# Optimization experiments

Hardware: AMD Instinct MI355X
Metric: run time of the kernel (lower is better)

## Reference

```python
import jax, jax.numpy as jnp
import numpy as np

B, C, H, W = 16, 1536, 32, 32
M = 64      # num_clusters
L = 128     # cluster_dim
G = 256     # token_dim
HID = 512
OT_ITERS = 3
EPS = 1e-6


def setup_inputs() -> dict:
    key = jax.random.key(0)
    ks = jax.random.split(key, 12)
    def w(k, shape, fan_in):
        return jax.random.normal(k, shape, jnp.float32) * (1.0 / np.sqrt(fan_in))
    return {
        'x': jax.random.normal(ks[0], (B, C, H, W), jnp.float32),
        't': jax.random.normal(ks[1], (B, C), jnp.float32),
        # token_features: Linear(C->512), ReLU, Linear(512->G)
        'Wt1': w(ks[2], (HID, C), C), 'bt1': jnp.zeros((HID,), jnp.float32),
        'Wt2': w(ks[3], (G, HID), HID), 'bt2': jnp.zeros((G,), jnp.float32),
        # cluster_features: 1x1 Conv(C->512), ReLU, 1x1 Conv(512->L)
        'Wc1': w(ks[4], (HID, C), C), 'bc1': jnp.zeros((HID,), jnp.float32),
        'Wc2': w(ks[5], (L, HID), HID), 'bc2': jnp.zeros((L,), jnp.float32),
        # score: 1x1 Conv(C->512), ReLU, 1x1 Conv(512->M)
        'Ws1': w(ks[6], (HID, C), C), 'bs1': jnp.zeros((HID,), jnp.float32),
        'Ws2': w(ks[7], (M, HID), HID), 'bs2': jnp.zeros((M,), jnp.float32),
        # temp_predictor: Conv1d(L->1, k=1)
        'Wtp': w(ks[8], (L,), L), 'btp': jnp.zeros((), jnp.float32),
        'dust_bin': jnp.asarray(1.0, jnp.float32),
        'burst_b': jnp.asarray(0.0, jnp.float32),
        'burst_p': jnp.asarray(1.0, jnp.float32),
        'lambda_discount': jnp.asarray(0.5, jnp.float32),
    }


def _log_optimal_transport(scores, alpha, iters):
    # scores: [B, m, n]; alpha: scalar dust-bin logit
    b, m, n = scores.shape
    Z0 = jnp.concatenate([scores, jnp.broadcast_to(alpha, (b, 1, n))], axis=1)  # [B, m+1, n]
    norm = -jnp.log(jnp.asarray(m + n, scores.dtype))
    log_mu = jnp.concatenate([jnp.full((m,), norm, scores.dtype),
                              (jnp.log(jnp.asarray(n, scores.dtype)) + norm)[None]])  # [m+1]
    log_nu = jnp.full((n,), norm, scores.dtype)
    u = jnp.zeros((b, m + 1), scores.dtype)
    v = jnp.zeros((b, n), scores.dtype)
    for _ in range(iters):
        u = log_mu - jax.nn.logsumexp(Z0 + v[:, None, :], axis=2)
        v = log_nu - jax.nn.logsumexp(Z0 + u[:, :, None], axis=1)
    return Z0 + u[:, :, None] + v[:, None, :] - norm


def _l2norm(a, axis):
    return a / jnp.maximum(jnp.linalg.norm(a, axis=axis, keepdims=True), 1e-12)


def _forward(x, t, Wt1, bt1, Wt2, bt2, Wc1, bc1, Wc2, bc2, Ws1, bs1, Ws2, bs2,
             Wtp, btp, dust_bin, burst_b, burst_p, lambda_discount):
    b, c, h, w = x.shape
    n = h * w
    xf = x.reshape(b, c, n)  # [B, C, N] (1x1 convs == per-pixel MLP)
    # cluster features f: [B, L, N]
    h1 = jax.nn.relu(jnp.einsum('bcn,oc->bon', xf, Wc1) + bc1[:, None])
    f = jnp.einsum('bhn,lh->bln', h1, Wc2) + bc2[:, None]
    # assignment scores p: [B, M, N]
    h2 = jax.nn.relu(jnp.einsum('bcn,oc->bon', xf, Ws1) + bs1[:, None])
    p = jnp.einsum('bhn,mh->bmn', h2, Ws2) + bs2[:, None]
    # global token: [B, G]
    tok = jax.nn.relu(t @ Wt1.T + bt1) @ Wt2.T + bt2
    # Sinkhorn OT soft assignment, drop dust bin row
    P = jnp.exp(_log_optimal_transport(p, dust_bin, OT_ITERS))[:, :-1, :]  # [B, M, N]
    # burst-aware weighting
    f_norm = _l2norm(f, axis=1)                                  # [B, L, N]
    T_i = jax.nn.softplus(jnp.einsum('bln,l->bn', f, Wtp) + btp)  # [B, N]
    sim = jnp.einsum('bli,blj->bij', f_norm, f_norm)              # [B, N, N]
    T_avg = (T_i[:, :, None] + T_i[:, None, :]) * 0.5
    burst_w = jax.nn.sigmoid(T_avg * sim + burst_b)
    discount = jnp.clip(jnp.sum(burst_w, axis=-1) ** burst_p, 1e-3, 1e3)  # [B, N]
    lam = jax.nn.sigmoid(lambda_discount)
    P_adj = (1.0 - lam) * P + lam * (P / (discount[:, None, :] + EPS))
    # local aggregation: (f[:, :, None, :] * P[:, None, :, :]).sum(-1) == batched matmul
    agg = jnp.einsum('bln,bmn->blm', f, P_adj)  # [B, L, M]
    agg = _l2norm(agg, axis=1).reshape(b, -1)   # [B, L*M]
    tok_n = _l2norm(tok, axis=-1)
    g = jnp.concatenate([tok_n, agg], axis=-1)  # [B, G + L*M]
    return _l2norm(g, axis=-1)


def reference(x, t, Wt1, bt1, Wt2, bt2, Wc1, bc1, Wc2, bc2, Ws1, bs1, Ws2, bs2,
              Wtp, btp, dust_bin, burst_b, burst_p, lambda_discount):
    return _forward(x, t, Wt1, bt1, Wt2, bt2, Wc1, bc1, Wc2, bc2, Ws1, bs1, Ws2, bs2,
                    Wtp, btp, dust_bin, burst_b, burst_p, lambda_discount)
```

## Files before the change

### kernel.cpp

```cpp
#include <hip/hip_runtime.h>
#include <math.h>

#define B_   16
#define C_   1536
#define N_   1024
#define M_   64
#define L_   128
#define G_   256
#define HID_ 512

typedef __attribute__((ext_vector_type(8))) short short8;
typedef __attribute__((ext_vector_type(4))) float floatx4;

__device__ __forceinline__ unsigned short f2bf_rne(float x) {
    unsigned u = __float_as_uint(x);
    unsigned r = u + 0x7fffu + ((u >> 16) & 1u);
    return (unsigned short)(r >> 16);
}
__device__ __forceinline__ unsigned pack_bf2(float lo, float hi) {
    unsigned a = __float_as_uint(lo) + 0x8000u;
    unsigned b = __float_as_uint(hi) + 0x8000u;
    return (a >> 16) | (b & 0xffff0000u);
}
__device__ __forceinline__ float bf2f(unsigned short u) {
    return __uint_as_float(((unsigned)u) << 16);
}
__device__ __forceinline__ void gl2lds16(const void* g, void* l) {
    __builtin_amdgcn_global_load_lds(
        (const __attribute__((address_space(1))) void*)g,
        (__attribute__((address_space(3))) void*)l, 16, 0, 0);
}

__global__ __launch_bounds__(256) void cast_w_kernel(
    const float* __restrict__ Wc1, const float* __restrict__ Ws1,
    const float* __restrict__ Wc2, const float* __restrict__ Ws2,
    unsigned short* __restrict__ Wbf, unsigned short* __restrict__ W2,
    float* __restrict__ agg, float* __restrict__ draw,
    float* __restrict__ rowsum)
{
    const int T1 = 1024 * 1536;
    const int T2 = 192 * 1024;
    int idx = blockIdx.x * 256 + threadIdx.x;
    if (idx < T1) {
        float v = (idx < 512 * 1536) ? Wc1[idx] : Ws1[idx - 512 * 1536];
        Wbf[idx] = f2bf_rne(v);
    } else if (idx < T1 + T2) {
        int i2 = idx - T1;
        int row = i2 >> 10, k = i2 & 1023;
        float v = 0.f;
        if (row < 128) { if (k < 512) v = Wc2[row * 512 + k]; }
        else           { if (k >= 512) v = Ws2[(row - 128) * 512 + (k - 512)]; }
        W2[i2] = f2bf_rne(v);
    } else {
        int zi = idx - (T1 + T2);
        if (zi < 131072) agg[zi] = 0.f;
        else if (zi < 131072 + 16384) draw[zi - 131072] = 0.f;
        else if (zi < 131072 + 16384 + 1040) rowsum[zi - 131072 - 16384] = 0.f;
    }
}

__global__ __launch_bounds__(256) void xt_kernel(
    const float* __restrict__ x, unsigned short* __restrict__ xT)
{
    __shared__ float Xs[64][65];
    const int t = threadIdx.x;
    const int n0 = blockIdx.x * 64, c0 = blockIdx.y * 64, b = blockIdx.z;
    const float* xb = x + (long)b * C_ * N_;
    #pragma unroll
    for (int it = 0; it < 16; ++it) {
        int idx = it * 256 + t, cr = idx >> 6, nc = idx & 63;
        Xs[cr][nc] = xb[(long)(c0 + cr) * N_ + n0 + nc];
    }
    __syncthreads();
    unsigned* xo = (unsigned*)(xT + (long)b * N_ * C_);
    #pragma unroll
    for (int it = 0; it < 8; ++it) {
        int idx = it * 256 + t, nr = idx >> 5, pc = idx & 31;
        xo[(long)(n0 + nr) * 768 + (c0 >> 1) + pc] =
            pack_bf2(Xs[2 * pc][nr], Xs[2 * pc + 1][nr]);
    }
}

__global__ __launch_bounds__(256, 2) void gemm1_kernel(
    const unsigned short* __restrict__ Wbf, const unsigned short* __restrict__ xT,
    const float* __restrict__ bc1, const float* __restrict__ bs1,
    unsigned short* __restrict__ hT)
{
    __shared__ unsigned short sh[8704];
    unsigned short* As = sh;
    unsigned short* Bs = sh + 4096;
    const int t = threadIdx.x;
    const int lane = t & 63, w = t >> 6;
    const int n0 = blockIdx.x * 128, o0 = blockIdx.y * 128, b = blockIdx.z;
    const unsigned short* xb = xT + (long)b * N_ * C_;

    const int wo = (w >> 1) * 64, wn = (w & 1) * 64;
    const int lrow = lane & 15, kgrp = lane >> 4;
    const int arow = t >> 2, acol = (t & 3) * 8;

    floatx4 acc[4][4];
    #pragma unroll
    for (int i = 0; i < 4; ++i)
        #pragma unroll
        for (int j = 0; j < 4; ++j) acc[i][j] = (floatx4)0.0f;

    for (int k0 = 0; k0 < C_; k0 += 32) {
        #pragma unroll
        for (int r = 0; r < 2; ++r)
            gl2lds16(Wbf + (long)(o0 + r * 64 + arow) * C_ + k0 + acol,
                     (char*)As + r * 4096 + t * 16);
        #pragma unroll
        for (int r = 0; r < 2; ++r)
            gl2lds16(xb + (long)(n0 + r * 64 + arow) * C_ + k0 + acol,
                     (char*)Bs + r * 4096 + t * 16);
        __syncthreads();
        short8 af[4], bfr[4];
        #pragma unroll
        for (int i = 0; i < 4; ++i)
            af[i] = *(const short8*)((const char*)As +
                        (wo + i * 16 + lrow) * 64 + kgrp * 16);
        #pragma unroll
        for (int j = 0; j < 4; ++j)
            bfr[j] = *(const short8*)((const char*)Bs +
                        (wn + j * 16 + lrow) * 64 + kgrp * 16);
        #pragma unroll
        for (int i = 0; i < 4; ++i)
            #pragma unroll
            for (int j = 0; j < 4; ++j)
                acc[i][j] = __builtin_amdgcn_mfma_f32_16x16x32_bf16(
                    af[i], bfr[j], acc[i][j], 0, 0, 0);
        __syncthreads();
    }

    const float* bias = (o0 < 512) ? bc1 : bs1;
    const int ob = (o0 < 512) ? o0 : o0 - 512;
    for (int half = 0; half < 2; ++half) {
        if ((w & 1) == half) {
            #pragma unroll
            for (int i = 0; i < 4; ++i) {
                int o_loc = wo + i * 16 + kgrp * 4;
                float b0 = bias[ob + o_loc + 0], b1 = bias[ob + o_loc + 1];
                float b2 = bias[ob + o_loc + 2], b3 = bias[ob + o_loc + 3];
                #pragma unroll
                for (int j = 0; j < 4; ++j) {
                    int n_loc = j * 16 + lrow;
                    float v0 = fmaxf(acc[i][j][0] + b0, 0.f);
                    float v1 = fmaxf(acc[i][j][1] + b1, 0.f);
                    float v2 = fmaxf(acc[i][j][2] + b2, 0.f);
                    float v3 = fmaxf(acc[i][j][3] + b3, 0.f);
                    uint2 pk;
                    pk.x = pack_bf2(v0, v1) & 0u;
                    pk.x = ((unsigned)f2bf_rne(v0)) | (((unsigned)f2bf_rne(v1)) << 16);
                    pk.y = ((unsigned)f2bf_rne(v2)) | (((unsigned)f2bf_rne(v3)) << 16);
                    *(uint2*)((char*)sh + n_loc * 272 + o_loc * 2) = pk;
                }
            }
        }
        __syncthreads();
        #pragma unroll
        for (int ps = 0; ps < 4; ++ps) {
            int n_loc = ps * 16 + (t >> 4);
            int o8 = (t & 15) * 8;
            uint4 q = *(const uint4*)((const char*)sh + n_loc * 272 + o8 * 2);
            *(uint4*)&hT[((long)b * N_ + n0 + half * 64 + n_loc) * 1024 + o0 + o8] = q;
        }
        __syncthreads();
    }
}

__global__ __launch_bounds__(256, 2) void gemm23_kernel(
    const unsigned short* __restrict__ W2, const unsigned short* __restrict__ hT,
    const float* __restrict__ bc2, const float* __restrict__ bs2,
    unsigned short* __restrict__ fbf, float* __restrict__ K,
    float* __restrict__ rowsum)
{
    __shared__ unsigned short As[64 * 32];
    __shared__ unsigned short Bs[128 * 32];
    const int t = threadIdx.x;
    const int lane = t & 63, w = t >> 6;
    const int n0 = blockIdx.x * 128, o0 = blockIdx.y * 64, b = blockIdx.z;
    const unsigned short* hTb = hT + (long)b * N_ * 1024;

    const int wo = (w >> 1) * 32, wn = (w & 1) * 64;
    const int lrow = lane & 15, kgrp = lane >> 4;
    const int arow = t >> 2, acol = (t & 3) * 8;

    floatx4 acc[2][4];
    #pragma unroll
    for (int i = 0; i < 2; ++i)
        #pragma unroll
        for (int j = 0; j < 4; ++j) acc[i][j] = (floatx4)0.0f;

    for (int k0 = 0; k0 < 1024; k0 += 32) {
        gl2lds16(W2 + (long)(o0 + arow) * 1024 + k0 + acol, (char*)As + t * 16);
        #pragma unroll
        for (int r = 0; r < 2; ++r)
            gl2lds16(hTb + (long)(n0 + r * 64 + arow) * 1024 + k0 + acol,
                     (char*)Bs + r * 4096 + t * 16);
        __syncthreads();
        short8 af[2], bfr[4];
        #pragma unroll
        for (int i = 0; i < 2; ++i)
            af[i] = *(const short8*)((const char*)As +
                        (wo + i * 16 + lrow) * 64 + kgrp * 16);
        #pragma unroll
        for (int j = 0; j < 4; ++j)
            bfr[j] = *(const short8*)((const char*)Bs +
                        (wn + j * 16 + lrow) * 64 + kgrp * 16);
        #pragma unroll
        for (int i = 0; i < 2; ++i)
            #pragma unroll
            for (int j = 0; j < 4; ++j)
                acc[i][j] = __builtin_amdgcn_mfma_f32_16x16x32_bf16(
                    af[i], bfr[j], acc[i][j], 0, 0, 0);
        __syncthreads();
    }

    if (o0 < 128) {
        #pragma unroll
        for (int i = 0; i < 2; ++i) {
            int o = o0 + wo + i * 16 + kgrp * 4;
            #pragma unroll
            for (int j = 0; j < 4; ++j) {
                int n = n0 + wn + j * 16 + lrow;
                #pragma unroll
                for (int r = 0; r < 4; ++r) {
                    int oo = o + r;
                    fbf[((long)b * L_ + oo) * N_ + n] =
                        f2bf_rne(acc[i][j][r] + bc2[oo]);
                }
            }
        }
    } else {
        float sloc[2][4] = {};
        #pragma unroll
        for (int i = 0; i < 2; ++i) {
            int m0 = wo + i * 16 + kgrp * 4;
            #pragma unroll
            for (int j = 0; j < 4; ++j) {
                int n = n0 + wn + j * 16 + lrow;
                #pragma unroll
                for (int r = 0; r < 4; ++r) {
                    int m = m0 + r;
                    float val = expf(acc[i][j][r] + bs2[m]);
                    K[((long)b * M_ + m) * N_ + n] = val;
                    sloc[i][r] += val;
                }
            }
        }
        #pragma unroll
        for (int i = 0; i < 2; ++i)
            #pragma unroll
            for (int r = 0; r < 4; ++r) {
                float s = sloc[i][r];
                #pragma unroll
                for (int off = 1; off < 16; off <<= 1) s += __shfl_xor(s, off);
                if (lrow == 0)
                    atomicAdd(&rowsum[b * 65 + wo + i * 16 + kgrp * 4 + r], s);
            }
    }
}

__global__ __launch_bounds__(256) void token1_kernel(
    const float* __restrict__ t_in, const float* __restrict__ Wt1,
    const float* __restrict__ bt1, float* __restrict__ hid)
{
    const int lane = threadIdx.x & 63, w = threadIdx.x >> 6;
    const int o = blockIdx.x * 4 + w, b = blockIdx.y;
    const float4* wr = (const float4*)(Wt1 + (long)o * C_);
    const float4* tb = (const float4*)(t_in + (long)b * C_);
    float acc = 0.f;
    #pragma unroll
    for (int i = 0; i < 6; ++i) {
        float4 a = wr[i * 64 + lane], tv = tb[i * 64 + lane];
        acc += a.x * tv.x + a.y * tv.y + a.z * tv.z + a.w * tv.w;
    }
    #pragma unroll
    for (int off = 1; off < 64; off <<= 1) acc += __shfl_xor(acc, off);
    if (lane == 0) hid[b * HID_ + o] = fmaxf(acc + bt1[o], 0.f);
}

__global__ __launch_bounds__(256) void token2_kernel(
    const float* __restrict__ hid, const float* __restrict__ Wt2,
    const float* __restrict__ bt2, float* __restrict__ tok)
{
    const int lane = threadIdx.x & 63, w = threadIdx.x >> 6;
    const int g = blockIdx.x * 4 + w, b = blockIdx.y;
    const float4* wr = (const float4*)(Wt2 + (long)g * HID_);
    const float4* hb = (const float4*)(hid + (long)b * HID_);
    float acc = 0.f;
    #pragma unroll
    for (int i = 0; i < 2; ++i) {
        float4 a = wr[i * 64 + lane], hv = hb[i * 64 + lane];
        acc += a.x * hv.x + a.y * hv.y + a.z * hv.z + a.w * hv.w;
    }
    #pragma unroll
    for (int off = 1; off < 64; off <<= 1) acc += __shfl_xor(acc, off);
    if (lane == 0) tok[b * G_ + g] = acc + bt2[g];
}

__global__ __launch_bounds__(256) void token3_kernel(
    const float* __restrict__ tok, float* __restrict__ tokn,
    const float* __restrict__ rowsum, const float* __restrict__ dust,
    float* __restrict__ avec)
{
    __shared__ float red[4];
    const int b = blockIdx.x, t = threadIdx.x;
    float v = tok[b * G_ + t];
    float ss = v * v;
    #pragma unroll
    for (int off = 1; off < 64; off <<= 1) ss += __shfl_xor(ss, off);
    if ((t & 63) == 0) red[t >> 6] = ss;
    if (t < 65) {
        float s  = (t < 64) ? rowsum[b * 65 + t] : 1024.f * expf(dust[0]);
        float mu = (t < 64) ? (1.f / 1088.f) : (1024.f / 1088.f);
        avec[b * 65 + t] = mu / s;
    }
    __syncthreads();
    float inv = 1.f / fmaxf(sqrtf(red[0] + red[1] + red[2] + red[3]), 1e-12f);
    tokn[b * G_ + t] = v * inv;
}

__global__ __launch_bounds__(256) void ku_kernel(
    const float* __restrict__ K, const float* __restrict__ dust,
    const float* __restrict__ bvec, float* __restrict__ avec)
{
    const int t = threadIdx.x, lane = t & 63, w = t >> 6;
    const int m = blockIdx.x * 4 + w, b = blockIdx.y;
    if (m > M_) return;
    const float* bv = bvec + b * N_;
    float s = 0.f;
    if (m < M_) {
        const float* row = K + ((long)b * M_ + m) * N_;
        #pragma unroll
        for (int i = 0; i < 16; ++i) {
            int n = i * 64 + lane;
            s += row[n] * bv[n];
        }
    } else {
        #pragma unroll
        for (int i = 0; i < 16; ++i) s += bv[i * 64 + lane];
        s *= expf(dust[0]);
    }
    #pragma unroll
    for (int off = 1; off < 64; off <<= 1) s += __shfl_xor(s, off);
    if (lane == 0) {
        float mu = (m < M_) ? (1.f / 1088.f) : (1024.f / 1088.f);
        avec[b * (M_ + 1) + m] = mu / s;
    }
}

__global__ __launch_bounds__(256) void kv_kernel(
    const float* __restrict__ K, const float* __restrict__ dust,
    const float* __restrict__ avec, float* __restrict__ bvec)
{
    __shared__ float a_s[M_ + 1];
    const int t = threadIdx.x, b = blockIdx.y;
    const int n = blockIdx.x * 256 + t;
    if (t < M_ + 1) a_s[t] = avec[b * (M_ + 1) + t];
    __syncthreads();
    float s = expf(dust[0]) * a_s[M_];
    const float* col = K + (long)b * M_ * N_ + n;
    #pragma unroll
    for (int m = 0; m < M_; ++m) s = fmaf(col[(long)m * N_], a_s[m], s);
    bvec[b * N_ + n] = (1.f / 1088.f) / s;
}

__global__ __launch_bounds__(256) void tnorm_kernel(
    const unsigned short* __restrict__ fbf, const float* __restrict__ Wtp,
    const float* __restrict__ btp, unsigned short* __restrict__ fnT,
    float* __restrict__ T)
{
    __shared__ float Ft[L_][65];
    __shared__ float invs[64];
    __shared__ float wtp_s[L_];
    const int b = blockIdx.y, n0 = blockIdx.x * 64, t = threadIdx.x;

    if (t < L_) wtp_s[t] = Wtp[t];
    #pragma unroll
    for (int it = 0; it < 4; ++it) {
        int l = it * 32 + (t >> 3), c0 = (t & 7) * 8;
        uint4 q = *(const uint4*)(fbf + ((long)(b * L_ + l)) * N_ + n0 + c0);
        Ft[l][c0 + 0] = bf2f((unsigned short)(q.x & 0xffff));
        Ft[l][c0 + 1] = bf2f((unsigned short)(q.x >> 16));
        Ft[l][c0 + 2] = bf2f((unsigned short)(q.y & 0xffff));
        Ft[l][c0 + 3] = bf2f((unsigned short)(q.y >> 16));
        Ft[l][c0 + 4] = bf2f((unsigned short)(q.z & 0xffff));
        Ft[l][c0 + 5] = bf2f((unsigned short)(q.z >> 16));
        Ft[l][c0 + 6] = bf2f((unsigned short)(q.w & 0xffff));
        Ft[l][c0 + 7] = bf2f((unsigned short)(q.w >> 16));
    }
    __syncthreads();
    if (t < 64) {
        float ss = 0.f, dot = 0.f;
        #pragma unroll
        for (int l = 0; l < L_; ++l) {
            float v = Ft[l][t];
            ss = fmaf(v, v, ss);
            dot = fmaf(v, wtp_s[l], dot);
        }
        invs[t] = 1.f / fmaxf(sqrtf(ss), 1e-12f);
        float xx = dot + btp[0];
        T[b * N_ + n0 + t] = (xx > 0.f) ? (xx + log1pf(expf(-xx)))
                                        : log1pf(expf(xx));
    }
    __syncthreads();
    unsigned* fo = (unsigned*)fnT;
    for (int it = 0; it < 16; ++it) {
        int idx = it * 256 + t;
        int nl = idx >> 6, jp = idx & 63;
        float inv = invs[nl];
        fo[(((long)b * N_ + n0 + nl) << 6) + jp] =
            pack_bf2(Ft[2 * jp][nl] * inv, Ft[2 * jp + 1][nl] * inv);
    }
}

__global__ __launch_bounds__(256) void sim_kernel(
    const unsigned short* __restrict__ fnT, const float* __restrict__ T,
    const float* __restrict__ bb, float* __restrict__ draw)
{
    __shared__ unsigned short As[64 * 136];
    __shared__ unsigned short Bs[64 * 136];
    __shared__ float Ti[64], Tj[64];
    const int b = blockIdx.z, i0 = blockIdx.y * 64, j0base = blockIdx.x * 256;
    const int t = threadIdx.x, lane = t & 63, w = t >> 6;
    const int lrow = lane & 15, kgrp = lane >> 4;
    const unsigned short* fb = fnT + (long)b * N_ * 128;
    const float burstb = bb[0];

    if (t < 64) Ti[t] = T[b * N_ + i0 + t];
    const int srow = t >> 4, scol = (t & 15) * 8;
    #pragma unroll
    for (int r = 0; r < 4; ++r) {
        uint4 av = *(const uint4*)(fb + (long)(i0 + r * 16 + srow) * 128 + scol);
        *(uint4*)((char*)As + (r * 16 + srow) * 272 + scol * 2) = av;
    }

    float rs[4] = {0.f, 0.f, 0.f, 0.f};
    for (int jj = 0; jj < 4; ++jj) {
        const int j0 = j0base + jj * 64;
        __syncthreads();
        #pragma unroll
        for (int r = 0; r < 4; ++r) {
            uint4 bv = *(const uint4*)(fb + (long)(j0 + r * 16 + srow) * 128 + scol);
            *(uint4*)((char*)Bs + (r * 16 + srow) * 272 + scol * 2) = bv;
        }
        if (t >= 64 && t < 128) Tj[t - 64] = T[b * N_ + j0 + (t - 64)];
        __syncthreads();

        floatx4 acc[4];
        #pragma unroll
        for (int j = 0; j < 4; ++j) acc[j] = (floatx4)0.0f;
        #pragma unroll
        for (int k0 = 0; k0 < 128; k0 += 32) {
            short8 af = *(const short8*)((const char*)As +
                            (w * 16 + lrow) * 272 + k0 * 2 + kgrp * 16);
            #pragma unroll
            for (int j = 0; j < 4; ++j) {
                short8 bf = *(const short8*)((const char*)Bs +
                                (j * 16 + lrow) * 272 + k0 * 2 + kgrp * 16);
                acc[j] = __builtin_amdgcn_mfma_f32_16x16x32_bf16(af, bf, acc[j], 0, 0, 0);
            }
        }
        #pragma unroll
        for (int j = 0; j < 4; ++j) {
            float Tjv = Tj[j * 16 + lrow];
            #pragma unroll
            for (int r = 0; r < 4; ++r) {
                float Tiv = Ti[w * 16 + kgrp * 4 + r];
                float xarg = 0.5f * (Tiv + Tjv) * acc[j][r] + burstb;
                rs[r] += 1.f / (1.f + expf(-xarg));
            }
        }
    }

    #pragma unroll
    for (int off = 1; off < 16; off <<= 1)
        #pragma unroll
        for (int r = 0; r < 4; ++r) rs[r] += __shfl_xor(rs[r], off);
    if (lrow == 0) {
        #pragma unroll
        for (int r = 0; r < 4; ++r)
            atomicAdd(&draw[b * N_ + i0 + w * 16 + kgrp * 4 + r], rs[r]);
    }
}

__global__ __launch_bounds__(256) void agg_kernel(
    const unsigned short* __restrict__ fbf, const float* __restrict__ K,
    const float* __restrict__ avec, const float* __restrict__ dust,
    const float* __restrict__ draw, const float* __restrict__ bp,
    const float* __restrict__ lamd, float* __restrict__ agg)
{
    __shared__ float fch[L_][65];
    __shared__ float Pch[M_][65];
    __shared__ float a_s[M_ + 1], cf[64];
    const int b = blockIdx.y, n0 = blockIdx.x * 64;
    const int t = threadIdx.x, tx = t & 15, ty = t >> 4;
    const float* Kb = K + (long)b * M_ * N_;

    if (t < M_ + 1) a_s[t] = avec[b * (M_ + 1) + t];

    #pragma unroll
    for (int it = 0; it < 4; ++it) {
        int l = it * 32 + (t >> 3), c0 = (t & 7) * 8;
        uint4 q = *(const uint4*)(fbf + ((long)(b * L_ + l)) * N_ + n0 + c0);
        fch[l][c0 + 0] = bf2f((unsigned short)(q.x & 0xffff));
        fch[l][c0 + 1] = bf2f((unsigned short)(q.x >> 16));
        fch[l][c0 + 2] = bf2f((unsigned short)(q.y & 0xffff));
        fch[l][c0 + 3] = bf2f((unsigned short)(q.y >> 16));
        fch[l][c0 + 4] = bf2f((unsigned short)(q.z & 0xffff));
        fch[l][c0 + 5] = bf2f((unsigned short)(q.z >> 16));
        fch[l][c0 + 6] = bf2f((unsigned short)(q.w & 0xffff));
        fch[l][c0 + 7] = bf2f((unsigned short)(q.w >> 16));
    }
    __syncthreads();
    for (int idx = t; idx < M_ * 64; idx += 256) {
        int m = idx >> 6, c = idx & 63;
        Pch[m][c] = Kb[(long)m * N_ + n0 + c] * a_s[m];
    }
    __syncthreads();

    if (t < 64) {
        float s = expf(dust[0]) * a_s[M_];
        #pragma unroll
        for (int m = 0; m < M_; ++m) s += Pch[m][t];
        float d = powf(draw[b * N_ + n0 + t], bp[0]);
        d = fminf(fmaxf(d, 1e-3f), 1e3f);
        float lam = 1.f / (1.f + expf(-lamd[0]));
        float wnv = (1.f - lam) + lam / (d + 1e-6f);
        cf[t] = wnv / s;
    }
    __syncthreads();

    float acc[8][4] = {};
    for (int n = 0; n < 64; ++n) {
        float cfn = cf[n];
        float fv[8], pv[4];
        #pragma unroll
        for (int i = 0; i < 8; ++i) fv[i] = fch[ty + 16 * i][n];
        #pragma unroll
        for (int j = 0; j < 4; ++j) pv[j] = Pch[tx * 4 + j][n] * cfn;
        #pragma unroll
        for (int i = 0; i < 8; ++i)
            #pragma unroll
            for (int j = 0; j < 4; ++j)
                acc[i][j] = fmaf(fv[i], pv[j], acc[i][j]);
    }
    #pragma unroll
    for (int i = 0; i < 8; ++i)
        #pragma unroll
        for (int j = 0; j < 4; ++j)
            atomicAdd(&agg[((long)b * L_ + (ty + 16 * i)) * M_ + tx * 4 + j],
                      acc[i][j]);
}

__global__ __launch_bounds__(256) void final_kernel(
    const float* __restrict__ tokn, const float* __restrict__ agg,
    float* __restrict__ out)
{
    __shared__ float invm[M_];
    __shared__ float red[4];
    __shared__ float s_invtot;
    const int b = blockIdx.x, t = threadIdx.x;
    const float* ab = agg + (long)b * L_ * M_;

    if (t < 64) {
        float ss = 0.f;
        for (int l = 0; l < L_; ++l) {
            float v = ab[l * M_ + t];
            ss = fmaf(v, v, ss);
        }
        invm[t] = 1.f / fmaxf(sqrtf(ss), 1e-12f);
    }
    __syncthreads();

    float part;
    {
        float tn = tokn[b * G_ + t];
        part = tn * tn;
    }
    for (int idx = t; idx < L_ * M_; idx += 256) {
        float v = ab[idx] * invm[idx & 63];
        part = fmaf(v, v, part);
    }
    for (int off = 32; off; off >>= 1) part += __shfl_down(part, off);
    if ((t & 63) == 0) red[t >> 6] = part;
    __syncthreads();
    if (t == 0)
        s_invtot = 1.f / fmaxf(sqrtf(red[0] + red[1] + red[2] + red[3]), 1e-12f);
    __syncthreads();

    const float invtot = s_invtot;
    float* ob = out + (long)b * (G_ + L_ * M_);
    ob[t] = tokn[b * G_ + t] * invtot;
    for (int idx = t; idx < L_ * M_; idx += 256)
        ob[G_ + idx] = ab[idx] * invm[idx & 63] * invtot;
}

extern "C" void kernel_launch(void* const* d_in, const int* in_sizes, int n_in,
                              void* d_out, int out_size, void* d_ws, size_t ws_size,
                              hipStream_t stream)
{
    const float* x    = (const float*)d_in[0];
    const float* t_in = (const float*)d_in[1];
    const float* Wt1  = (const float*)d_in[2];
    const float* bt1  = (const float*)d_in[3];
    const float* Wt2  = (const float*)d_in[4];
    const float* bt2  = (const float*)d_in[5];
    const float* Wc1  = (const float*)d_in[6];
    const float* bc1  = (const float*)d_in[7];
    const float* Wc2  = (const float*)d_in[8];
    const float* bc2  = (const float*)d_in[9];
    const float* Ws1  = (const float*)d_in[10];
    const float* bs1  = (const float*)d_in[11];
    const float* Ws2  = (const float*)d_in[12];
    const float* bs2  = (const float*)d_in[13];
    const float* Wtp  = (const float*)d_in[14];
    const float* btp  = (const float*)d_in[15];
    const float* dust = (const float*)d_in[16];
    const float* bb   = (const float*)d_in[17];
    const float* bp   = (const float*)d_in[18];
    const float* lamd = (const float*)d_in[19];

    char* wsb = (char*)d_ws;
    unsigned short* xT  = (unsigned short*)wsb;
    unsigned short* fbf = (unsigned short*)(wsb + 0);
    float* K    = (float*)(wsb + 4194304);
    unsigned short* fnT = (unsigned short*)(wsb + 8388608);
    float* hid  = (float*)(wsb + 12582912);
    float* tok  = (float*)(wsb + 12615680);
    float* tokn = (float*)(wsb + 12632064);
    float* T    = (float*)(wsb + 12648448);
    float* avec = (float*)(wsb + 12713984);
    float* bvec = (float*)(wsb + 12718144);
    unsigned short* hT  = (unsigned short*)(wsb + 50331648);
    unsigned short* Wbf = (unsigned short*)(wsb + 83886080);
    unsigned short* W2  = (unsigned short*)(wsb + 87031808);
    float* draw   = (float*)(wsb + 87425024);
    float* agg    = (float*)(wsb + 87490560);
    float* rowsum = (float*)(wsb + 88014848);
    float* out  = (float*)d_out;

    cast_w_kernel<<<7493, 256, 0, stream>>>(Wc1, Ws1, Wc2, Ws2, Wbf, W2,
                                            agg, draw, rowsum);

    xt_kernel    <<<dim3(16, 24, 16), 256, 0, stream>>>(x, xT);
    gemm1_kernel <<<dim3(8, 8, 16), 256, 0, stream>>>(Wbf, xT, bc1, bs1, hT);
    gemm23_kernel<<<dim3(8, 3, 16), 256, 0, stream>>>(W2, hT, bc2, bs2,
                                                      fbf, K, rowsum);

    token1_kernel<<<dim3(128, 16), 256, 0, stream>>>(t_in, Wt1, bt1, hid);
    token2_kernel<<<dim3(64, 16), 256, 0, stream>>>(hid, Wt2, bt2, tok);
    token3_kernel<<<16, 256, 0, stream>>>(tok, tokn, rowsum, dust, avec);

    kv_kernel<<<dim3(4, 16), 256, 0, stream>>>(K, dust, avec, bvec);
    ku_kernel<<<dim3(17, 16), 256, 0, stream>>>(K, dust, bvec, avec);
    kv_kernel<<<dim3(4, 16), 256, 0, stream>>>(K, dust, avec, bvec);
    ku_kernel<<<dim3(17, 16), 256, 0, stream>>>(K, dust, bvec, avec);

    tnorm_kernel<<<dim3(16, 16), 256, 0, stream>>>(fbf, Wtp, btp, fnT, T);
    sim_kernel  <<<dim3(4, 16, 16), 256, 0, stream>>>(fnT, T, bb, draw);
    agg_kernel  <<<dim3(16, 16), 256, 0, stream>>>(fbf, K, avec, dust,
                                                   draw, bp, lamd, agg);
    final_kernel<<<16, 256, 0, stream>>>(tokn, agg, out);
}
```

Measured before the change: 399.4 us.

## Merge prep, token MLP, Sinkhorn and tnorm kernels to cut launches

Folds the x transpose into the weight-cast kernel as one launch. Merges the token MLP, the two Sinkhorn iterations and the tnorm kernel into a single heterogeneous kernel whose blocks are split by block index, which removes many small launches and the intermediate global buffers. The GEMM launch bounds are raised to 3 waves per SIMD. In exchange, the token MLP now runs on only 16 blocks and each Sinkhorn batch on one block, which serialises that work and can lengthen the critical path. The higher occupancy hint may also force register spills.

```diff
diff --git a/kernel.cpp b/kernel.cpp
--- a/kernel.cpp
+++ b/kernel.cpp
@@ -31,57 +31,57 @@
         (__attribute__((address_space(3))) void*)l, 16, 0, 0);
 }
 
-__global__ __launch_bounds__(256) void cast_w_kernel(
+__global__ __launch_bounds__(256) void prep_kernel(
+    const float* __restrict__ x, unsigned short* __restrict__ xT,
     const float* __restrict__ Wc1, const float* __restrict__ Ws1,
     const float* __restrict__ Wc2, const float* __restrict__ Ws2,
     unsigned short* __restrict__ Wbf, unsigned short* __restrict__ W2,
     float* __restrict__ agg, float* __restrict__ draw,
     float* __restrict__ rowsum)
 {
-    const int T1 = 1024 * 1536;
-    const int T2 = 192 * 1024;
-    int idx = blockIdx.x * 256 + threadIdx.x;
-    if (idx < T1) {
-        float v = (idx < 512 * 1536) ? Wc1[idx] : Ws1[idx - 512 * 1536];
-        Wbf[idx] = f2bf_rne(v);
-    } else if (idx < T1 + T2) {
-        int i2 = idx - T1;
-        int row = i2 >> 10, k = i2 & 1023;
-        float v = 0.f;
-        if (row < 128) { if (k < 512) v = Wc2[row * 512 + k]; }
-        else           { if (k >= 512) v = Ws2[(row - 128) * 512 + (k - 512)]; }
-        W2[i2] = f2bf_rne(v);
+    __shared__ float Xs[64][65];
+    const int bid = blockIdx.x, t = threadIdx.x;
+    if (bid < 6144) {
+        const int b = bid / 384, rem = bid % 384;
+        const int c0 = (rem >> 4) * 64, n0 = (rem & 15) * 64;
+        const float* xb = x + (long)b * C_ * N_;
+        #pragma unroll
+        for (int it = 0; it < 16; ++it) {
+            int idx = it * 256 + t, cr = idx >> 6, nc = idx & 63;
+            Xs[cr][nc] = xb[(long)(c0 + cr) * N_ + n0 + nc];
+        }
+        __syncthreads();
+        unsigned* xo = (unsigned*)(xT + (long)b * N_ * C_);
+        #pragma unroll
+        for (int it = 0; it < 8; ++it) {
+            int idx = it * 256 + t, nr = idx >> 5, pc = idx & 31;
+            xo[(long)(n0 + nr) * 768 + (c0 >> 1) + pc] =
+                pack_bf2(Xs[2 * pc][nr], Xs[2 * pc + 1][nr]);
+        }
     } else {
-        int zi = idx - (T1 + T2);
-        if (zi < 131072) agg[zi] = 0.f;
-        else if (zi < 131072 + 16384) draw[zi - 131072] = 0.f;
-        else if (zi < 131072 + 16384 + 1040) rowsum[zi - 131072 - 16384] = 0.f;
-    }
-}
-
-__global__ __launch_bounds__(256) void xt_kernel(
-    const float* __restrict__ x, unsigned short* __restrict__ xT)
-{
-    __shared__ float Xs[64][65];
-    const int t = threadIdx.x;
-    const int n0 = blockIdx.x * 64, c0 = blockIdx.y * 64, b = blockIdx.z;
-    const float* xb = x + (long)b * C_ * N_;
-    #pragma unroll
-    for (int it = 0; it < 16; ++it) {
-        int idx = it * 256 + t, cr = idx >> 6, nc = idx & 63;
-        Xs[cr][nc] = xb[(long)(c0 + cr) * N_ + n0 + nc];
-    }
-    __syncthreads();
-    unsigned* xo = (unsigned*)(xT + (long)b * N_ * C_);
-    #pragma unroll
-    for (int it = 0; it < 8; ++it) {
-        int idx = it * 256 + t, nr = idx >> 5, pc = idx & 31;
-        xo[(long)(n0 + nr) * 768 + (c0 >> 1) + pc] =
-            pack_bf2(Xs[2 * pc][nr], Xs[2 * pc + 1][nr]);
-    }
-}
-
-__global__ __launch_bounds__(256, 2) void gemm1_kernel(
+        const int T1 = 1024 * 1536;
+        const int T2 = 192 * 1024;
+        int idx = (bid - 6144) * 256 + t;
+        if (idx < T1) {
+            float v = (idx < 512 * 1536) ? Wc1[idx] : Ws1[idx - 512 * 1536];
+            Wbf[idx] = f2bf_rne(v);
+        } else if (idx < T1 + T2) {
+            int i2 = idx - T1;
+            int row = i2 >> 10, k = i2 & 1023;
+            float v = 0.f;
+            if (row < 128) { if (k < 512) v = Wc2[row * 512 + k]; }
+            else           { if (k >= 512) v = Ws2[(row - 128) * 512 + (k - 512)]; }
+            W2[i2] = f2bf_rne(v);
+        } else {
+            int zi = idx - (T1 + T2);
+            if (zi < 131072) agg[zi] = 0.f;
+            else if (zi < 131072 + 16384) draw[zi - 131072] = 0.f;
+            else if (zi < 131072 + 16384 + 1040) rowsum[zi - 131072 - 16384] = 0.f;
+        }
+    }
+}
+
+__global__ __launch_bounds__(256, 3) void gemm1_kernel(
     const unsigned short* __restrict__ Wbf, const unsigned short* __restrict__ xT,
     const float* __restrict__ bc1, const float* __restrict__ bs1,
     unsigned short* __restrict__ hT)
@@ -149,7 +149,6 @@
                     float v2 = fmaxf(acc[i][j][2] + b2, 0.f);
                     float v3 = fmaxf(acc[i][j][3] + b3, 0.f);
                     uint2 pk;
-                    pk.x = pack_bf2(v0, v1) & 0u;
                     pk.x = ((unsigned)f2bf_rne(v0)) | (((unsigned)f2bf_rne(v1)) << 16);
                     pk.y = ((unsigned)f2bf_rne(v2)) | (((unsigned)f2bf_rne(v3)) << 16);
                     *(uint2*)((char*)sh + n_loc * 272 + o_loc * 2) = pk;
@@ -168,7 +167,7 @@
     }
 }
 
-__global__ __launch_bounds__(256, 2) void gemm23_kernel(
+__global__ __launch_bounds__(256, 3) void gemm23_kernel(
     const unsigned short* __restrict__ W2, const unsigned short* __restrict__ hT,
     const float* __restrict__ bc2, const float* __restrict__ bs2,
     unsigned short* __restrict__ fbf, float* __restrict__ K,
@@ -261,157 +260,160 @@
     }
 }
 
-__global__ __launch_bounds__(256) void token1_kernel(
-    const float* __restrict__ t_in, const float* __restrict__ Wt1,
-    const float* __restrict__ bt1, float* __restrict__ hid)
-{
-    const int lane = threadIdx.x & 63, w = threadIdx.x >> 6;
-    const int o = blockIdx.x * 4 + w, b = blockIdx.y;
-    const float4* wr = (const float4*)(Wt1 + (long)o * C_);
-    const float4* tb = (const float4*)(t_in + (long)b * C_);
-    float acc = 0.f;
-    #pragma unroll
-    for (int i = 0; i < 6; ++i) {
-        float4 a = wr[i * 64 + lane], tv = tb[i * 64 + lane];
-        acc += a.x * tv.x + a.y * tv.y + a.z * tv.z + a.w * tv.w;
-    }
-    #pragma unroll
-    for (int off = 1; off < 64; off <<= 1) acc += __shfl_xor(acc, off);
-    if (lane == 0) hid[b * HID_ + o] = fmaxf(acc + bt1[o], 0.f);
-}
-
-__global__ __launch_bounds__(256) void token2_kernel(
-    const float* __restrict__ hid, const float* __restrict__ Wt2,
-    const float* __restrict__ bt2, float* __restrict__ tok)
-{
-    const int lane = threadIdx.x & 63, w = threadIdx.x >> 6;
-    const int g = blockIdx.x * 4 + w, b = blockIdx.y;
-    const float4* wr = (const float4*)(Wt2 + (long)g * HID_);
-    const float4* hb = (const float4*)(hid + (long)b * HID_);
-    float acc = 0.f;
-    #pragma unroll
-    for (int i = 0; i < 2; ++i) {
-        float4 a = wr[i * 64 + lane], hv = hb[i * 64 + lane];
-        acc += a.x * hv.x + a.y * hv.y + a.z * hv.z + a.w * hv.w;
-    }
-    #pragma unroll
-    for (int off = 1; off < 64; off <<= 1) acc += __shfl_xor(acc, off);
-    if (lane == 0) tok[b * G_ + g] = acc + bt2[g];
-}
-
-__global__ __launch_bounds__(256) void token3_kernel(
-    const float* __restrict__ tok, float* __restrict__ tokn,
-    const float* __restrict__ rowsum, const float* __restrict__ dust,
-    float* __restrict__ avec)
-{
-    __shared__ float red[4];
-    const int b = blockIdx.x, t = threadIdx.x;
-    float v = tok[b * G_ + t];
-    float ss = v * v;
-    #pragma unroll
-    for (int off = 1; off < 64; off <<= 1) ss += __shfl_xor(ss, off);
-    if ((t & 63) == 0) red[t >> 6] = ss;
-    if (t < 65) {
-        float s  = (t < 64) ? rowsum[b * 65 + t] : 1024.f * expf(dust[0]);
-        float mu = (t < 64) ? (1.f / 1088.f) : (1024.f / 1088.f);
-        avec[b * 65 + t] = mu / s;
-    }
-    __syncthreads();
-    float inv = 1.f / fmaxf(sqrtf(red[0] + red[1] + red[2] + red[3]), 1e-12f);
-    tokn[b * G_ + t] = v * inv;
-}
-
-__global__ __launch_bounds__(256) void ku_kernel(
-    const float* __restrict__ K, const float* __restrict__ dust,
-    const float* __restrict__ bvec, float* __restrict__ avec)
-{
-    const int t = threadIdx.x, lane = t & 63, w = t >> 6;
-    const int m = blockIdx.x * 4 + w, b = blockIdx.y;
-    if (m > M_) return;
-    const float* bv = bvec + b * N_;
-    float s = 0.f;
-    if (m < M_) {
-        const float* row = K + ((long)b * M_ + m) * N_;
-        #pragma unroll
-        for (int i = 0; i < 16; ++i) {
-            int n = i * 64 + lane;
-            s += row[n] * bv[n];
-        }
-    } else {
-        #pragma unroll
-        for (int i = 0; i < 16; ++i) s += bv[i * 64 + lane];
-        s *= expf(dust[0]);
-    }
-    #pragma unroll
-    for (int off = 1; off < 64; off <<= 1) s += __shfl_xor(s, off);
-    if (lane == 0) {
-        float mu = (m < M_) ? (1.f / 1088.f) : (1024.f / 1088.f);
-        avec[b * (M_ + 1) + m] = mu / s;
-    }
-}
-
-__global__ __launch_bounds__(256) void kv_kernel(
-    const float* __restrict__ K, const float* __restrict__ dust,
-    const float* __restrict__ avec, float* __restrict__ bvec)
-{
-    __shared__ float a_s[M_ + 1];
-    const int t = threadIdx.x, b = blockIdx.y;
-    const int n = blockIdx.x * 256 + t;
-    if (t < M_ + 1) a_s[t] = avec[b * (M_ + 1) + t];
-    __syncthreads();
-    float s = expf(dust[0]) * a_s[M_];
-    const float* col = K + (long)b * M_ * N_ + n;
-    #pragma unroll
-    for (int m = 0; m < M_; ++m) s = fmaf(col[(long)m * N_], a_s[m], s);
-    bvec[b * N_ + n] = (1.f / 1088.f) / s;
-}
-
-__global__ __launch_bounds__(256) void tnorm_kernel(
+__global__ __launch_bounds__(256) void mid_kernel(
     const unsigned short* __restrict__ fbf, const float* __restrict__ Wtp,
     const float* __restrict__ btp, unsigned short* __restrict__ fnT,
-    float* __restrict__ T)
-{
-    __shared__ float Ft[L_][65];
-    __shared__ float invs[64];
-    __shared__ float wtp_s[L_];
-    const int b = blockIdx.y, n0 = blockIdx.x * 64, t = threadIdx.x;
-
-    if (t < L_) wtp_s[t] = Wtp[t];
-    #pragma unroll
-    for (int it = 0; it < 4; ++it) {
-        int l = it * 32 + (t >> 3), c0 = (t & 7) * 8;
-        uint4 q = *(const uint4*)(fbf + ((long)(b * L_ + l)) * N_ + n0 + c0);
-        Ft[l][c0 + 0] = bf2f((unsigned short)(q.x & 0xffff));
-        Ft[l][c0 + 1] = bf2f((unsigned short)(q.x >> 16));
-        Ft[l][c0 + 2] = bf2f((unsigned short)(q.y & 0xffff));
-        Ft[l][c0 + 3] = bf2f((unsigned short)(q.y >> 16));
-        Ft[l][c0 + 4] = bf2f((unsigned short)(q.z & 0xffff));
-        Ft[l][c0 + 5] = bf2f((unsigned short)(q.z >> 16));
-        Ft[l][c0 + 6] = bf2f((unsigned short)(q.w & 0xffff));
-        Ft[l][c0 + 7] = bf2f((unsigned short)(q.w >> 16));
-    }
-    __syncthreads();
-    if (t < 64) {
-        float ss = 0.f, dot = 0.f;
-        #pragma unroll
-        for (int l = 0; l < L_; ++l) {
-            float v = Ft[l][t];
-            ss = fmaf(v, v, ss);
-            dot = fmaf(v, wtp_s[l], dot);
-        }
-        invs[t] = 1.f / fmaxf(sqrtf(ss), 1e-12f);
-        float xx = dot + btp[0];
-        T[b * N_ + n0 + t] = (xx > 0.f) ? (xx + log1pf(expf(-xx)))
-                                        : log1pf(expf(xx));
-    }
-    __syncthreads();
-    unsigned* fo = (unsigned*)fnT;
-    for (int it = 0; it < 16; ++it) {
-        int idx = it * 256 + t;
-        int nl = idx >> 6, jp = idx & 63;
-        float inv = invs[nl];
-        fo[(((long)b * N_ + n0 + nl) << 6) + jp] =
-            pack_bf2(Ft[2 * jp][nl] * inv, Ft[2 * jp + 1][nl] * inv);
+    float* __restrict__ T,
+    const float* __restrict__ t_in, const float* __restrict__ Wt1,
+    const float* __restrict__ bt1,  const float* __restrict__ Wt2,
+    const float* __restrict__ bt2,  float* __restrict__ tokn,
+    const float* __restrict__ K, const float* __restrict__ rowsum,
+    const float* __restrict__ dust, float* __restrict__ avec)
+{
+    __shared__ float smem[8512];
+    const int bid = blockIdx.x, t = threadIdx.x;
+    const int lane = t & 63, w = t >> 6;
+
+    if (bid < 256) {
+        const int b = bid >> 4, n0 = (bid & 15) << 6;
+        float (*Ft)[65] = (float(*)[65])smem;
+        float* invs  = smem + 8320;
+        float* wtp_s = smem + 8384;
+        if (t < L_) wtp_s[t] = Wtp[t];
+        #pragma unroll
+        for (int it = 0; it < 4; ++it) {
+            int l = it * 32 + (t >> 3), c0 = (t & 7) * 8;
+            uint4 q = *(const uint4*)(fbf + ((long)(b * L_ + l)) * N_ + n0 + c0);
+            Ft[l][c0 + 0] = bf2f((unsigned short)(q.x & 0xffff));
+            Ft[l][c0 + 1] = bf2f((unsigned short)(q.x >> 16));
+            Ft[l][c0 + 2] = bf2f((unsigned short)(q.y & 0xffff));
+            Ft[l][c0 + 3] = bf2f((unsigned short)(q.y >> 16));
+            Ft[l][c0 + 4] = bf2f((unsigned short)(q.z & 0xffff));
+            Ft[l][c0 + 5] = bf2f((unsigned short)(q.z >> 16));
+            Ft[l][c0 + 6] = bf2f((unsigned short)(q.w & 0xffff));
+            Ft[l][c0 + 7] = bf2f((unsigned short)(q.w >> 16));
+        }
+        __syncthreads();
+        if (t < 64) {
+            float ss = 0.f, dot = 0.f;
+            #pragma unroll
+            for (int l = 0; l < L_; ++l) {
+                float v = Ft[l][t];
+                ss = fmaf(v, v, ss);
+                dot = fmaf(v, wtp_s[l], dot);
+            }
+            invs[t] = 1.f / fmaxf(sqrtf(ss), 1e-12f);
+            float xx = dot + btp[0];
+            T[b * N_ + n0 + t] = (xx > 0.f) ? (xx + log1pf(expf(-xx)))
+                                            : log1pf(expf(xx));
+        }
+        __syncthreads();
+        unsigned* fo = (unsigned*)fnT;
+        for (int it = 0; it < 16; ++it) {
+            int idx = it * 256 + t;
+            int nl = idx >> 6, jp = idx & 63;
+            float inv = invs[nl];
+            fo[(((long)b * N_ + n0 + nl) << 6) + jp] =
+                pack_bf2(Ft[2 * jp][nl] * inv, Ft[2 * jp + 1][nl] * inv);
+        }
+    } else if (bid < 272) {
+        const int b = bid - 256;
+        float* tb   = smem;
+        float* hid  = smem + 1536;
+        float* tokl = smem + 2048;
+        float* red  = smem + 2304;
+        for (int i = t; i < C_; i += 256) tb[i] = t_in[b * C_ + i];
+        __syncthreads();
+        const float4* tb4 = (const float4*)tb;
+        for (int oi = 0; oi < 128; ++oi) {
+            int o = w * 128 + oi;
+            const float4* wr = (const float4*)(Wt1 + (long)o * C_);
+            float acc = 0.f;
+            #pragma unroll
+            for (int i = 0; i < 6; ++i) {
+                float4 a = wr[i * 64 + lane], tv = tb4[i * 64 + lane];
+                acc += a.x * tv.x + a.y * tv.y + a.z * tv.z + a.w * tv.w;
+            }
+            #pragma unroll
+            for (int off = 1; off < 64; off <<= 1) acc += __shfl_xor(acc, off);
+            if (lane == 0) hid[o] = fmaxf(acc + bt1[o], 0.f);
+        }
+        __syncthreads();
+        const float4* hb4 = (const float4*)hid;
+        for (int gi = 0; gi < 64; ++gi) {
+            int g = w * 64 + gi;
+            const float4* wr = (const float4*)(Wt2 + (long)g * HID_);
+            float acc = 0.f;
+            #pragma unroll
+            for (int i = 0; i < 2; ++i) {
+                float4 a = wr[i * 64 + lane], hv = hb4[i * 64 + lane];
+                acc += a.x * hv.x + a.y * hv.y + a.z * hv.z + a.w * hv.w;
+            }
+            #pragma unroll
+            for (int off = 1; off < 64; off <<= 1) acc += __shfl_xor(acc, off);
+            if (lane == 0) tokl[g] = acc + bt2[g];
+        }
+        __syncthreads();
+        float v = tokl[t];
+        float ss = v * v;
+        #pragma unroll
+        for (int off = 1; off < 64; off <<= 1) ss += __shfl_xor(ss, off);
+        if (lane == 0) red[w] = ss;
+        __syncthreads();
+        float inv = 1.f / fmaxf(sqrtf(red[0] + red[1] + red[2] + red[3]), 1e-12f);
+        tokn[b * G_ + t] = v * inv;
+    } else {
+        const int b = bid - 272;
+        float* b_s = smem;
+        float* a_s = smem + 1024;
+        const float ea = expf(dust[0]);
+        if (t < 65) {
+            float s  = (t < 64) ? rowsum[b * 65 + t] : 1024.f * ea;
+            float mu = (t < 64) ? (1.f / 1088.f) : (1024.f / 1088.f);
+            a_s[t] = mu / s;
+        }
+        __syncthreads();
+        const float* Kb = K + (long)b * M_ * N_;
+        for (int iter = 0; iter < 2; ++iter) {
+            float s4[4];
+            #pragma unroll
+            for (int q = 0; q < 4; ++q) s4[q] = ea * a_s[64];
+            for (int m = 0; m < 64; ++m) {
+                float am = a_s[m];
+                const float* Kr = Kb + (long)m * N_;
+                #pragma unroll
+                for (int q = 0; q < 4; ++q)
+                    s4[q] = fmaf(Kr[q * 256 + t], am, s4[q]);
+            }
+            __syncthreads();
+            #pragma unroll
+            for (int q = 0; q < 4; ++q)
+                b_s[q * 256 + t] = (1.f / 1088.f) / s4[q];
+            __syncthreads();
+            for (int mi = 0; mi < 16; ++mi) {
+                int m = w * 16 + mi;
+                const float* Kr = Kb + (long)m * N_;
+                float s = 0.f;
+                #pragma unroll
+                for (int i = 0; i < 16; ++i) {
+                    int n = i * 64 + lane;
+                    s = fmaf(Kr[n], b_s[n], s);
+                }
+                #pragma unroll
+                for (int off = 1; off < 64; off <<= 1) s += __shfl_xor(s, off);
+                if (lane == 0) a_s[m] = (1.f / 1088.f) / s;
+            }
+            if (w == 3) {
+                float s = 0.f;
+                #pragma unroll
+                for (int i = 0; i < 16; ++i) s += b_s[i * 64 + lane];
+                #pragma unroll
+                for (int off = 1; off < 64; off <<= 1) s += __shfl_xor(s, off);
+                if (lane == 0) a_s[64] = (1024.f / 1088.f) / (ea * s);
+            }
+            __syncthreads();
+        }
+        if (t < 65) avec[b * 65 + t] = a_s[t];
     }
 }
 
@@ -627,12 +629,9 @@
     unsigned short* fbf = (unsigned short*)(wsb + 0);
     float* K    = (float*)(wsb + 4194304);
     unsigned short* fnT = (unsigned short*)(wsb + 8388608);
-    float* hid  = (float*)(wsb + 12582912);
-    float* tok  = (float*)(wsb + 12615680);
-    float* tokn = (float*)(wsb + 12632064);
-    float* T    = (float*)(wsb + 12648448);
-    float* avec = (float*)(wsb + 12713984);
-    float* bvec = (float*)(wsb + 12718144);
+    float* tokn = (float*)(wsb + 12582912);
+    float* T    = (float*)(wsb + 12599296);
+    float* avec = (float*)(wsb + 12664832);
     unsigned short* hT  = (unsigned short*)(wsb + 50331648);
     unsigned short* Wbf = (unsigned short*)(wsb + 83886080);
     unsigned short* W2  = (unsigned short*)(wsb + 87031808);
@@ -641,26 +640,16 @@
     float* rowsum = (float*)(wsb + 88014848);
     float* out  = (float*)d_out;
 
-    cast_w_kernel<<<7493, 256, 0, stream>>>(Wc1, Ws1, Wc2, Ws2, Wbf, W2,
-                                            agg, draw, rowsum);
-
-    xt_kernel    <<<dim3(16, 24, 16), 256, 0, stream>>>(x, xT);
+    prep_kernel  <<<13637, 256, 0, stream>>>(x, xT, Wc1, Ws1, Wc2, Ws2,
+                                             Wbf, W2, agg, draw, rowsum);
     gemm1_kernel <<<dim3(8, 8, 16), 256, 0, stream>>>(Wbf, xT, bc1, bs1, hT);
     gemm23_kernel<<<dim3(8, 3, 16), 256, 0, stream>>>(W2, hT, bc2, bs2,
                                                       fbf, K, rowsum);
-
-    token1_kernel<<<dim3(128, 16), 256, 0, stream>>>(t_in, Wt1, bt1, hid);
-    token2_kernel<<<dim3(64, 16), 256, 0, stream>>>(hid, Wt2, bt2, tok);
-    token3_kernel<<<16, 256, 0, stream>>>(tok, tokn, rowsum, dust, avec);
-
-    kv_kernel<<<dim3(4, 16), 256, 0, stream>>>(K, dust, avec, bvec);
-    ku_kernel<<<dim3(17, 16), 256, 0, stream>>>(K, dust, bvec, avec);
-    kv_kernel<<<dim3(4, 16), 256, 0, stream>>>(K, dust, avec, bvec);
-    ku_kernel<<<dim3(17, 16), 256, 0, stream>>>(K, dust, bvec, avec);
-
-    tnorm_kernel<<<dim3(16, 16), 256, 0, stream>>>(fbf, Wtp, btp, fnT, T);
-    sim_kernel  <<<dim3(4, 16, 16), 256, 0, stream>>>(fnT, T, bb, draw);
-    agg_kernel  <<<dim3(16, 16), 256, 0, stream>>>(fbf, K, avec, dust,
-                                                   draw, bp, lamd, agg);
-    final_kernel<<<16, 256, 0, stream>>>(tokn, agg, out);
-}
+    mid_kernel   <<<288, 256, 0, stream>>>(fbf, Wtp, btp, fnT, T,
+                                           t_in, Wt1, bt1, Wt2, bt2, tokn,
+                                           K, rowsum, dust, avec);
+    sim_kernel   <<<dim3(4, 16, 16), 256, 0, stream>>>(fnT, T, bb, draw);
+    agg_kernel   <<<dim3(16, 16), 256, 0, stream>>>(fbf, K, avec, dust,
+                                                    draw, bp, lamd, agg);
+    final_kernel <<<16, 256, 0, stream>>>(tokn, agg, out);
+}
```

Result: slower. 579.7 us (+45.1%).
